# Optimization experiments

Hardware: AMD Instinct MI355X
Metric: run time of the kernel (lower is better)

Reference implementation:

```python
import jax, jax.numpy as jnp
import numpy as np

DIM, HID, E, K = 1024, 2048, 8, 2


def setup_inputs() -> dict:
    key = jax.random.key(0)
    ks = jax.random.split(key, 5)
    x = jax.random.normal(ks[0], (2, 2048, DIM), dtype=jnp.float32)
    # router (torch zero-inits; use small random so routing is non-degenerate)
    router_w = jax.random.normal(ks[1], (DIM, E), dtype=jnp.float32) * 0.02
    router_b = jnp.zeros((E,), dtype=jnp.float32)
    # stacked expert params: w12 [E, dim, 2*hidden], w3 [E, hidden, dim]
    w12 = jax.random.normal(ks[2], (E, DIM, 2 * HID), dtype=jnp.float32) * 0.02
    w3 = jax.random.normal(ks[3], (E, HID, DIM), dtype=jnp.float32) * 0.02
    return {"x": x, "router_w": router_w, "router_b": router_b, "w12": w12, "w3": w3}


def reference(x, router_w, router_b, w12, w3):
    # router logits [b, s, e]; eval mode -> no jitter noise
    logits = jnp.einsum("bsd,de->bse", x, router_w) + router_b
    scores = jax.nn.sigmoid(logits)
    top_v, top_i = jax.lax.top_k(scores, K)            # [b, s, k]
    rw = top_v / (jnp.sum(top_v, axis=-1, keepdims=True) + 1e-6)
    # per-token combine weight for each expert (0 if not routed)
    oh = jax.nn.one_hot(top_i, E, dtype=x.dtype)       # [b, s, k, e]
    cw = jnp.einsum("bsk,bske->bse", rw, oh)           # [b, s, e]
    # dense all-expert SwiGLU (matches original masked-dense math)
    x12 = jnp.einsum("bsd,edh->bseh", x, w12)          # [b, s, e, 2H]
    x1, x2 = jnp.split(x12, 2, axis=-1)
    h = jax.nn.silu(x1) * x2                           # [b, s, e, H]
    eout = jnp.einsum("bseh,ehd->bsed", h, w3)         # [b, s, e, dim]
    out = jnp.einsum("bsed,bse->bsd", eout, cw)
    aux_loss = 0.01 * jnp.mean(logits ** 2)
    return out, aux_loss
```

## Files before the change

### kernel.cpp

```cpp
#include <hip/hip_runtime.h>
#include <hip/hip_bf16.h>
#include <stdint.h>

typedef __bf16 bf16_t;
typedef __bf16 bf16x8 __attribute__((ext_vector_type(8)));
typedef __bf16 bf16x4 __attribute__((ext_vector_type(4)));
typedef float f32x4 __attribute__((ext_vector_type(4)));

#define T_TOK 4096
#define DIM   1024
#define HID   2048
#define NE    8
#define MAXT  72

__device__ __forceinline__ void gload_lds16(const void* g, void* l) {
  __builtin_amdgcn_global_load_lds(
      (const __attribute__((address_space(1))) unsigned int*)g,
      (__attribute__((address_space(3))) unsigned int*)l, 16, 0, 0);
}

__device__ __forceinline__ void wt_tile(const float* __restrict__ in,
                                        bf16_t* __restrict__ out,
                                        int K, int N, int e, int ky, int nx,
                                        bf16_t (*tileT)[264]) {
  const size_t eoff = (size_t)e * K * N;
  const int k0 = ky * 256, n0 = nx * 128;
  const int tid = threadIdx.x;
  const int kl = tid >> 5;
  const int n4 = (tid & 31) * 4;
#pragma unroll
  for (int it = 0; it < 32; ++it) {
    int k = it * 8 + kl;
    float4 v = *(const float4*)(in + eoff + (size_t)(k0 + k) * N + n0 + n4);
    tileT[n4 + 0][k] = (bf16_t)v.x;
    tileT[n4 + 1][k] = (bf16_t)v.y;
    tileT[n4 + 2][k] = (bf16_t)v.z;
    tileT[n4 + 3][k] = (bf16_t)v.w;
  }
  __syncthreads();
  const int kc = (tid & 31) * 8;
#pragma unroll
  for (int it = 0; it < 16; ++it) {
    int n = it * 8 + kl;
    bf16x8 o = *(const bf16x8*)(&tileT[n][kc]);
    *(bf16x8*)(out + eoff + (size_t)(n0 + n) * K + k0 + kc) = o;
  }
}

__global__ __launch_bounds__(256) void k_prep(
    const float* __restrict__ x, const float* __restrict__ rw,
    const float* __restrict__ rb, const float* __restrict__ w12,
    const float* __restrict__ w3, bf16_t* __restrict__ xb,
    bf16_t* __restrict__ w12t, bf16_t* __restrict__ w3t,
    int* __restrict__ counts, int* __restrict__ top_i, float* __restrict__ top_w,
    float* __restrict__ aux) {
  __shared__ bf16_t tileT[128][264];
  const int b = blockIdx.x;
  if (b < 1024) {
    int e = b >> 7, rem = b & 127;
    wt_tile(w12, w12t, DIM, 2 * HID, e, rem >> 5, rem & 31, tileT);
    return;
  }
  if (b < 1536) {
    int lb = b - 1024;
    int e = lb >> 6, rem = lb & 63;
    wt_tile(w3, w3t, HID, DIM, e, rem >> 3, rem & 7, tileT);
    return;
  }
  int t = (b - 1536) * 4 + (threadIdx.x >> 6);
  int lane = threadIdx.x & 63;
  const float* xt = x + (size_t)t * DIM;
  float acc[8] = {0.f,0.f,0.f,0.f,0.f,0.f,0.f,0.f};
#pragma unroll
  for (int it = 0; it < 4; ++it) {
    int i = (it * 64 + lane) * 4;
    float4 xv = *(const float4*)(xt + i);
    bf16x4 o;
    o[0] = (bf16_t)xv.x; o[1] = (bf16_t)xv.y; o[2] = (bf16_t)xv.z; o[3] = (bf16_t)xv.w;
    *(bf16x4*)(xb + (size_t)t * DIM + i) = o;
#pragma unroll
    for (int c = 0; c < 4; ++c) {
      float v = (c == 0) ? xv.x : (c == 1) ? xv.y : (c == 2) ? xv.z : xv.w;
      float4 r0 = *(const float4*)(rw + (size_t)(i + c) * 8);
      float4 r1 = *(const float4*)(rw + (size_t)(i + c) * 8 + 4);
      acc[0] += v * r0.x; acc[1] += v * r0.y; acc[2] += v * r0.z; acc[3] += v * r0.w;
      acc[4] += v * r1.x; acc[5] += v * r1.y; acc[6] += v * r1.z; acc[7] += v * r1.w;
    }
  }
#pragma unroll
  for (int m = 32; m >= 1; m >>= 1) {
#pragma unroll
    for (int e = 0; e < 8; ++e) acc[e] += __shfl_xor(acc[e], m, 64);
  }
  if (lane == 0) {
    float s[8]; float sumsq = 0.f;
#pragma unroll
    for (int e = 0; e < 8; ++e) {
      float lg = acc[e] + rb[e];
      sumsq += lg * lg;
      s[e] = 1.f / (1.f + __expf(-lg));
    }
    int i1 = 0;
#pragma unroll
    for (int e = 1; e < 8; ++e) if (s[e] > s[i1]) i1 = e;
    int i2 = (i1 == 0) ? 1 : 0;
#pragma unroll
    for (int e = 0; e < 8; ++e) if (e != i1 && s[e] > s[i2]) i2 = e;
    float v1 = s[i1], v2 = s[i2];
    float den = v1 + v2 + 1e-6f;
    top_i[2 * t]     = i1; top_i[2 * t + 1] = i2;
    top_w[2 * t]     = v1 / den;
    top_w[2 * t + 1] = v2 / den;
    atomicAdd(&counts[i1], 1);
    atomicAdd(&counts[i2], 1);
    atomicAdd(aux, 0.01f * sumsq * (1.f / 32768.f));
  }
}

__global__ void k_plan(const int* __restrict__ counts, int* __restrict__ base,
                       int* __restrict__ tile_e, int* __restrict__ tile_m0) {
  if (threadIdx.x == 0) {
    int s = 0, nt = 0;
    for (int e = 0; e < NE; ++e) {
      base[e] = s;
      int c = counts[e];
      for (int m0 = 0; m0 < c; m0 += 128) { tile_e[nt] = e; tile_m0[nt] = m0; ++nt; }
      s += c;
    }
    for (; nt < MAXT; ++nt) tile_e[nt] = -1;
  }
}

__global__ __launch_bounds__(256) void k_gather(const int* __restrict__ top_i,
    const float* __restrict__ top_w, const int* __restrict__ base,
    int* __restrict__ fill, int* __restrict__ slot_token, float* __restrict__ slot_wt,
    int* __restrict__ slot_of) {
  int t = blockIdx.x * 256 + threadIdx.x;
  if (t >= T_TOK) return;
#pragma unroll
  for (int j = 0; j < 2; ++j) {
    int e = top_i[2 * t + j];
    int p = atomicAdd(&fill[e], 1);
    int g = base[e] + p;
    slot_token[g] = t;
    slot_wt[g]    = top_w[2 * t + j];
    slot_of[2 * t + j] = g;
  }
}

__global__ __launch_bounds__(256) void k_gemm1(
    const bf16_t* __restrict__ xb, const bf16_t* __restrict__ w12t,
    const int* __restrict__ counts, const int* __restrict__ base,
    const int* __restrict__ tile_e, const int* __restrict__ tile_m0,
    const int* __restrict__ slot_token, bf16_t* __restrict__ h) {
  const int e = tile_e[blockIdx.y];
  if (e < 0) return;
  const int m0  = tile_m0[blockIdx.y];
  const int cnt = counts[e];
  const int bas = base[e];
  const int n0  = blockIdx.x * 64;
  const bf16_t* W1 = w12t + (size_t)e * (4096u * 1024u) + (size_t)n0 * 1024u;
  const bf16_t* W2 = W1 + (size_t)2048 * 1024;

  __shared__ bf16_t sA[2][128 * 64];
  __shared__ bf16_t sB1[2][64 * 64];
  __shared__ bf16_t sB2[2][64 * 64];

  const int tid = threadIdx.x, lane = tid & 63, wid = tid >> 6;
  const int wr = wid >> 1, wc = wid & 1;
  const int lr = lane >> 3, sw = (lane & 7) ^ lr;

  int tokA[4];
#pragma unroll
  for (int i = 0; i < 4; ++i) {
    int row = m0 + wid * 32 + i * 8 + lr;
    tokA[i] = slot_token[bas + (row < cnt ? row : cnt - 1)];
  }

  auto stage = [&](int p, int k0) {
#pragma unroll
    for (int i = 0; i < 4; ++i)
      gload_lds16(xb + (size_t)tokA[i] * DIM + k0 + sw * 8,
                  &sA[p][(wid * 32 + i * 8) * 64]);
#pragma unroll
    for (int i = 0; i < 2; ++i) {
      int n = wid * 16 + i * 8 + lr;
      gload_lds16(W1 + (size_t)n * 1024 + k0 + sw * 8, &sB1[p][(wid * 16 + i * 8) * 64]);
      gload_lds16(W2 + (size_t)n * 1024 + k0 + sw * 8, &sB2[p][(wid * 16 + i * 8) * 64]);
    }
  };

  f32x4 acc1[4][2] = {};
  f32x4 acc2[4][2] = {};

  stage(0, 0);
  stage(1, 64);

  const int NT = DIM / 64;
  for (int t = 0; t < NT; ++t) {
    const int p = t & 1;
    if (t + 2 < NT) asm volatile("s_waitcnt vmcnt(8)" ::: "memory");
    else            asm volatile("s_waitcnt vmcnt(0)" ::: "memory");
    __builtin_amdgcn_s_barrier();
    asm volatile("" ::: "memory");
    __builtin_amdgcn_s_setprio(1);
#pragma unroll
    for (int kk = 0; kk < 2; ++kk) {
      const int g = kk * 4 + (lane >> 4);
      bf16x8 a[4], b1[2], b2[2];
#pragma unroll
      for (int mf = 0; mf < 4; ++mf) {
        int r = wr * 64 + mf * 16 + (lane & 15);
        a[mf] = *(const bf16x8*)(&sA[p][r * 64 + ((g ^ (r & 7)) << 3)]);
      }
#pragma unroll
      for (int nf = 0; nf < 2; ++nf) {
        int n = wc * 32 + nf * 16 + (lane & 15);
        b1[nf] = *(const bf16x8*)(&sB1[p][n * 64 + ((g ^ (n & 7)) << 3)]);
        b2[nf] = *(const bf16x8*)(&sB2[p][n * 64 + ((g ^ (n & 7)) << 3)]);
      }
#pragma unroll
      for (int mf = 0; mf < 4; ++mf)
#pragma unroll
        for (int nf = 0; nf < 2; ++nf) {
          acc1[mf][nf] = __builtin_amdgcn_mfma_f32_16x16x32_bf16(a[mf], b1[nf], acc1[mf][nf], 0, 0, 0);
          acc2[mf][nf] = __builtin_amdgcn_mfma_f32_16x16x32_bf16(a[mf], b2[nf], acc2[mf][nf], 0, 0, 0);
        }
    }
    __builtin_amdgcn_s_setprio(0);
    __builtin_amdgcn_sched_barrier(0);
    __builtin_amdgcn_s_barrier();
    asm volatile("" ::: "memory");
    if (t + 2 < NT) stage(p, (t + 2) * 64);
  }

#pragma unroll
  for (int mf = 0; mf < 4; ++mf)
#pragma unroll
    for (int r = 0; r < 4; ++r) {
      int m = wr * 64 + mf * 16 + ((lane >> 4) << 2) + r;
      if (m0 + m < cnt) {
        size_t rowoff = (size_t)(bas + m0 + m) * HID + n0;
#pragma unroll
        for (int nf = 0; nf < 2; ++nf) {
          int col = wc * 32 + nf * 16 + (lane & 15);
          float d1 = acc1[mf][nf][r], d2 = acc2[mf][nf][r];
          h[rowoff + col] = (bf16_t)((d1 / (1.f + __expf(-d1))) * d2);
        }
      }
    }
}

__global__ __launch_bounds__(256) void k_gemm2(
    const bf16_t* __restrict__ h, const bf16_t* __restrict__ w3t,
    const int* __restrict__ counts, const int* __restrict__ base,
    const int* __restrict__ tile_e, const int* __restrict__ tile_m0,
    const float* __restrict__ slot_wt, bf16_t* __restrict__ eout) {
  const int e = tile_e[blockIdx.y];
  if (e < 0) return;
  const int m0  = tile_m0[blockIdx.y];
  const int cnt = counts[e];
  const int bas = base[e];
  const int n0 = blockIdx.x * 128;
  const bf16_t* W = w3t + (size_t)e * (1024u * 2048u);

  __shared__ bf16_t sA[2][128 * 64];
  __shared__ bf16_t sB[2][128 * 64];

  const int tid = threadIdx.x, lane = tid & 63, wid = tid >> 6;
  const int wr = wid >> 1, wc = wid & 1;
  const int lr = lane >> 3, sw = (lane & 7) ^ lr;

  int rowA[4];
#pragma unroll
  for (int i = 0; i < 4; ++i) {
    int row = m0 + wid * 32 + i * 8 + lr;
    rowA[i] = bas + (row < cnt ? row : cnt - 1);
  }

  auto stage = [&](int p, int k0) {
#pragma unroll
    for (int i = 0; i < 4; ++i) {
      int rr = wid * 32 + i * 8;
      gload_lds16(h + (size_t)rowA[i] * HID + k0 + sw * 8, &sA[p][rr * 64]);
      gload_lds16(W + (size_t)(n0 + rr + lr) * 2048 + k0 + sw * 8, &sB[p][rr * 64]);
    }
  };

  f32x4 acc[4][4] = {};

  stage(0, 0);
  stage(1, 64);

  const int NT = HID / 64;
  for (int t = 0; t < NT; ++t) {
    const int p = t & 1;
    if (t + 2 < NT) asm volatile("s_waitcnt vmcnt(8)" ::: "memory");
    else            asm volatile("s_waitcnt vmcnt(0)" ::: "memory");
    __builtin_amdgcn_s_barrier();
    asm volatile("" ::: "memory");
    __builtin_amdgcn_s_setprio(1);
#pragma unroll
    for (int kk = 0; kk < 2; ++kk) {
      const int g = kk * 4 + (lane >> 4);
      bf16x8 a[4], b[4];
#pragma unroll
      for (int mf = 0; mf < 4; ++mf) {
        int r = wr * 64 + mf * 16 + (lane & 15);
        a[mf] = *(const bf16x8*)(&sA[p][r * 64 + ((g ^ (r & 7)) << 3)]);
      }
#pragma unroll
      for (int nf = 0; nf < 4; ++nf) {
        int n = wc * 64 + nf * 16 + (lane & 15);
        b[nf] = *(const bf16x8*)(&sB[p][n * 64 + ((g ^ (n & 7)) << 3)]);
      }
#pragma unroll
      for (int mf = 0; mf < 4; ++mf)
#pragma unroll
        for (int nf = 0; nf < 4; ++nf)
          acc[mf][nf] = __builtin_amdgcn_mfma_f32_16x16x32_bf16(a[mf], b[nf], acc[mf][nf], 0, 0, 0);
    }
    __builtin_amdgcn_s_setprio(0);
    __builtin_amdgcn_sched_barrier(0);
    __builtin_amdgcn_s_barrier();
    asm volatile("" ::: "memory");
    if (t + 2 < NT) stage(p, (t + 2) * 64);
  }

#pragma unroll
  for (int mf = 0; mf < 4; ++mf)
#pragma unroll
    for (int r = 0; r < 4; ++r) {
      int m = wr * 64 + mf * 16 + ((lane >> 4) << 2) + r;
      if (m0 + m < cnt) {
        int gs = bas + m0 + m;
        float wt = slot_wt[gs];
        size_t o = (size_t)gs * DIM + n0;
#pragma unroll
        for (int nf = 0; nf < 4; ++nf) {
          int col = wc * 64 + nf * 16 + (lane & 15);
          eout[o + col] = (bf16_t)(acc[mf][nf][r] * wt);
        }
      }
    }
}

__global__ __launch_bounds__(256) void k_combine(const bf16_t* __restrict__ eout,
    const int* __restrict__ slot_of, float* __restrict__ out) {
  const int t = blockIdx.x;
  const int c = threadIdx.x * 4;
  const int g0 = slot_of[2 * t], g1 = slot_of[2 * t + 1];
  bf16x4 a = *(const bf16x4*)(eout + (size_t)g0 * DIM + c);
  bf16x4 b = *(const bf16x4*)(eout + (size_t)g1 * DIM + c);
  float4 o;
  o.x = (float)a[0] + (float)b[0];
  o.y = (float)a[1] + (float)b[1];
  o.z = (float)a[2] + (float)b[2];
  o.w = (float)a[3] + (float)b[3];
  *(float4*)(out + (size_t)t * DIM + c) = o;
}

extern "C" void kernel_launch(void* const* d_in, const int* in_sizes, int n_in,
                              void* d_out, int out_size, void* d_ws, size_t ws_size,
                              hipStream_t stream) {
  const float* x   = (const float*)d_in[0];
  const float* rw  = (const float*)d_in[1];
  const float* rb  = (const float*)d_in[2];
  const float* w12 = (const float*)d_in[3];
  const float* w3  = (const float*)d_in[4];
  float* out = (float*)d_out;
  float* aux = out + (size_t)T_TOK * DIM;

  char* ws = (char*)d_ws;
  int*   counts     = (int*)(ws + 0);
  int*   fill       = (int*)(ws + 64);
  int*   base       = (int*)(ws + 128);
  int*   top_i      = (int*)(ws + 4096);
  float* top_w      = (float*)(ws + 4096 + 32768);
  int*   slot_token = (int*)(ws + 4096 + 65536);
  float* slot_wt    = (float*)(ws + 4096 + 98304);
  int*   slot_of    = (int*)(ws + 4096 + 131072);
  int*   tile_e     = (int*)(ws + 4096 + 163840);
  int*   tile_m0    = (int*)(ws + 4096 + 164352);
  bf16_t* xb        = (bf16_t*)(ws + 262144);
  bf16_t* h         = (bf16_t*)(ws + 262144 + 8388608);
  bf16_t* w12t      = (bf16_t*)(ws + 262144 + 8388608 + 33554432);
  bf16_t* w3t       = (bf16_t*)((char*)w12t + 67108864);
  bf16_t* eout      = w12t;

  hipMemsetAsync(ws, 0, 256, stream);
  hipMemsetAsync(aux, 0, sizeof(float), stream);

  k_prep<<<dim3(2560), dim3(256), 0, stream>>>(x, rw, rb, w12, w3, xb, w12t, w3t,
                                               counts, top_i, top_w, aux);
  k_plan<<<dim3(1), dim3(64), 0, stream>>>(counts, base, tile_e, tile_m0);
  k_gather<<<dim3(T_TOK / 256), dim3(256), 0, stream>>>(top_i, top_w, base, fill,
                                                        slot_token, slot_wt, slot_of);
  k_gemm1<<<dim3(HID / 64, MAXT), dim3(256), 0, stream>>>(
      xb, w12t, counts, base, tile_e, tile_m0, slot_token, h);
  k_gemm2<<<dim3(DIM / 128, MAXT), dim3(256), 0, stream>>>(
      h, w3t, counts, base, tile_e, tile_m0, slot_wt, eout);
  k_combine<<<dim3(T_TOK), dim3(256), 0, stream>>>(eout, slot_of, out);
}
```

Baseline: 372.0 us.

## Fuse w12 conversion into first expert GEMM with per-tile readiness flags

The w12 fp32-to-bf16 transpose moves out of the prep kernel and into the first GEMM launch as its first 32 rows of blocks. Each of these blocks bumps a per-(expert, column-chunk) flag with release semantics when it finishes. GEMM blocks spin on the flags covering their W1 and W2 columns before loading, so conversion of later weight tiles can overlap GEMM work on tiles already converted. The cost is spin-waiting, which can deadlock or stall if GEMM blocks get scheduled ahead of the converter blocks they wait on, plus a larger shared LDS footprint.

```diff
diff --git a/kernel.cpp b/kernel.cpp
--- a/kernel.cpp
+++ b/kernel.cpp
@@ -47,27 +47,20 @@
   }
 }
 
-__global__ __launch_bounds__(256) void k_prep(
+__global__ __launch_bounds__(256) void k_prepA(
     const float* __restrict__ x, const float* __restrict__ rw,
-    const float* __restrict__ rb, const float* __restrict__ w12,
-    const float* __restrict__ w3, bf16_t* __restrict__ xb,
-    bf16_t* __restrict__ w12t, bf16_t* __restrict__ w3t,
+    const float* __restrict__ rb, const float* __restrict__ w3,
+    bf16_t* __restrict__ xb, bf16_t* __restrict__ w3t,
     int* __restrict__ counts, int* __restrict__ top_i, float* __restrict__ top_w,
     float* __restrict__ aux) {
   __shared__ bf16_t tileT[128][264];
   const int b = blockIdx.x;
-  if (b < 1024) {
-    int e = b >> 7, rem = b & 127;
-    wt_tile(w12, w12t, DIM, 2 * HID, e, rem >> 5, rem & 31, tileT);
-    return;
-  }
-  if (b < 1536) {
-    int lb = b - 1024;
-    int e = lb >> 6, rem = lb & 63;
+  if (b < 512) {
+    int e = b >> 6, rem = b & 63;
     wt_tile(w3, w3t, HID, DIM, e, rem >> 3, rem & 7, tileT);
     return;
   }
-  int t = (b - 1536) * 4 + (threadIdx.x >> 6);
+  int t = (b - 512) * 4 + (threadIdx.x >> 6);
   int lane = threadIdx.x & 63;
   const float* xt = x + (size_t)t * DIM;
   float acc[8] = {0.f,0.f,0.f,0.f,0.f,0.f,0.f,0.f};
@@ -148,25 +141,55 @@
   }
 }
 
-__global__ __launch_bounds__(256) void k_gemm1(
-    const bf16_t* __restrict__ xb, const bf16_t* __restrict__ w12t,
+__global__ __launch_bounds__(256) void k_fused1(
+    const float* __restrict__ w12, bf16_t* __restrict__ w12t,
+    int* __restrict__ wflag,
+    const bf16_t* __restrict__ xb,
     const int* __restrict__ counts, const int* __restrict__ base,
     const int* __restrict__ tile_e, const int* __restrict__ tile_m0,
     const int* __restrict__ slot_token, bf16_t* __restrict__ h) {
-  const int e = tile_e[blockIdx.y];
+  __shared__ __align__(16) char lds_raw[67584];
+  const int tid = threadIdx.x;
+
+  if (blockIdx.y < 32) {
+    int id = blockIdx.y * 32 + blockIdx.x;
+    int e = id >> 7, rem = id & 127;
+    int ky = rem >> 5, nx = rem & 31;
+    wt_tile(w12, w12t, DIM, 2 * HID, e, ky, nx, (bf16_t(*)[264])lds_raw);
+    __threadfence();
+    __syncthreads();
+    if (tid == 0) __hip_atomic_fetch_add(&wflag[e * 32 + nx], 1,
+                                         __ATOMIC_RELEASE, __HIP_MEMORY_SCOPE_AGENT);
+    return;
+  }
+
+  const int ty = blockIdx.y - 32;
+  const int e = tile_e[ty];
   if (e < 0) return;
-  const int m0  = tile_m0[blockIdx.y];
+  const int m0  = tile_m0[ty];
   const int cnt = counts[e];
   const int bas = base[e];
   const int n0  = blockIdx.x * 64;
+
+  if (tid == 0) {
+    const int f1 = e * 32 + (n0 >> 7);
+    const int f2 = e * 32 + ((n0 + 2048) >> 7);
+    while (__hip_atomic_load(&wflag[f1], __ATOMIC_ACQUIRE, __HIP_MEMORY_SCOPE_AGENT) < 4 ||
+           __hip_atomic_load(&wflag[f2], __ATOMIC_ACQUIRE, __HIP_MEMORY_SCOPE_AGENT) < 4)
+      __builtin_amdgcn_s_sleep(2);
+  }
+  __syncthreads();
+  __threadfence();
+  asm volatile("" ::: "memory");
+
   const bf16_t* W1 = w12t + (size_t)e * (4096u * 1024u) + (size_t)n0 * 1024u;
   const bf16_t* W2 = W1 + (size_t)2048 * 1024;
 
-  __shared__ bf16_t sA[2][128 * 64];
-  __shared__ bf16_t sB1[2][64 * 64];
-  __shared__ bf16_t sB2[2][64 * 64];
-
-  const int tid = threadIdx.x, lane = tid & 63, wid = tid >> 6;
+  bf16_t* sA  = (bf16_t*)lds_raw;
+  bf16_t* sB1 = sA + 2 * 128 * 64;
+  bf16_t* sB2 = sB1 + 2 * 64 * 64;
+
+  const int lane = tid & 63, wid = tid >> 6;
   const int wr = wid >> 1, wc = wid & 1;
   const int lr = lane >> 3, sw = (lane & 7) ^ lr;
 
@@ -181,12 +204,12 @@
 #pragma unroll
     for (int i = 0; i < 4; ++i)
       gload_lds16(xb + (size_t)tokA[i] * DIM + k0 + sw * 8,
-                  &sA[p][(wid * 32 + i * 8) * 64]);
+                  sA + p * 8192 + (wid * 32 + i * 8) * 64);
 #pragma unroll
     for (int i = 0; i < 2; ++i) {
       int n = wid * 16 + i * 8 + lr;
-      gload_lds16(W1 + (size_t)n * 1024 + k0 + sw * 8, &sB1[p][(wid * 16 + i * 8) * 64]);
-      gload_lds16(W2 + (size_t)n * 1024 + k0 + sw * 8, &sB2[p][(wid * 16 + i * 8) * 64]);
+      gload_lds16(W1 + (size_t)n * 1024 + k0 + sw * 8, sB1 + p * 4096 + (wid * 16 + i * 8) * 64);
+      gload_lds16(W2 + (size_t)n * 1024 + k0 + sw * 8, sB2 + p * 4096 + (wid * 16 + i * 8) * 64);
     }
   };
 
@@ -211,13 +234,13 @@
 #pragma unroll
       for (int mf = 0; mf < 4; ++mf) {
         int r = wr * 64 + mf * 16 + (lane & 15);
-        a[mf] = *(const bf16x8*)(&sA[p][r * 64 + ((g ^ (r & 7)) << 3)]);
+        a[mf] = *(const bf16x8*)(sA + p * 8192 + r * 64 + ((g ^ (r & 7)) << 3));
       }
 #pragma unroll
       for (int nf = 0; nf < 2; ++nf) {
         int n = wc * 32 + nf * 16 + (lane & 15);
-        b1[nf] = *(const bf16x8*)(&sB1[p][n * 64 + ((g ^ (n & 7)) << 3)]);
-        b2[nf] = *(const bf16x8*)(&sB2[p][n * 64 + ((g ^ (n & 7)) << 3)]);
+        b1[nf] = *(const bf16x8*)(sB1 + p * 4096 + n * 64 + ((g ^ (n & 7)) << 3));
+        b2[nf] = *(const bf16x8*)(sB2 + p * 4096 + n * 64 + ((g ^ (n & 7)) << 3));
       }
 #pragma unroll
       for (int mf = 0; mf < 4; ++mf)
@@ -375,6 +398,7 @@
   int*   counts     = (int*)(ws + 0);
   int*   fill       = (int*)(ws + 64);
   int*   base       = (int*)(ws + 128);
+  int*   wflag      = (int*)(ws + 2048);
   int*   top_i      = (int*)(ws + 4096);
   float* top_w      = (float*)(ws + 4096 + 32768);
   int*   slot_token = (int*)(ws + 4096 + 65536);
@@ -388,16 +412,16 @@
   bf16_t* w3t       = (bf16_t*)((char*)w12t + 67108864);
   bf16_t* eout      = w12t;
 
-  hipMemsetAsync(ws, 0, 256, stream);
+  hipMemsetAsync(ws, 0, 4096, stream);
   hipMemsetAsync(aux, 0, sizeof(float), stream);
 
-  k_prep<<<dim3(2560), dim3(256), 0, stream>>>(x, rw, rb, w12, w3, xb, w12t, w3t,
-                                               counts, top_i, top_w, aux);
+  k_prepA<<<dim3(1536), dim3(256), 0, stream>>>(x, rw, rb, w3, xb, w3t,
+                                                counts, top_i, top_w, aux);
   k_plan<<<dim3(1), dim3(64), 0, stream>>>(counts, base, tile_e, tile_m0);
   k_gather<<<dim3(T_TOK / 256), dim3(256), 0, stream>>>(top_i, top_w, base, fill,
                                                         slot_token, slot_wt, slot_of);
-  k_gemm1<<<dim3(HID / 64, MAXT), dim3(256), 0, stream>>>(
-      xb, w12t, counts, base, tile_e, tile_m0, slot_token, h);
+  k_fused1<<<dim3(32, 32 + MAXT), dim3(256), 0, stream>>>(
+      w12, w12t, wflag, xb, counts, base, tile_e, tile_m0, slot_token, h);
   k_gemm2<<<dim3(DIM / 128, MAXT), dim3(256), 0, stream>>>(
       h, w3t, counts, base, tile_e, tile_m0, slot_wt, eout);
   k_combine<<<dim3(T_TOK), dim3(256), 0, stream>>>(eout, slot_of, out);
```

Measured after the change: 872.0 us. +134.4%, slower.
